# Kernel tuning notes

Measured on AMD Instinct MI355X. Metric: run time of the kernel, lower is better.

The kernel has to match this reference:

```python
import jax, jax.numpy as jnp
import numpy as np

FPS = [32, 64, 128, 256]
SPATIAL = [(32, 32, 32), (16, 16, 16), (8, 8, 8), (4, 4, 4)]
N_FEAT = 512
B = 2
HEAD_DIM = 16
EPS = 1e-5


def setup_inputs() -> dict:
    key = jax.random.key(0)
    ks = iter(jax.random.split(key, 64))
    inp = {}
    for i, (c, (h, w, z)) in enumerate(zip(FPS, SPATIAL)):
        inp[f"x{i}"] = jax.random.normal(next(ks), (B, c, h, w, z), jnp.float32)
        inp[f"f{i}"] = jax.random.normal(next(ks), (N_FEAT, c), jnp.float32)
        inp[f"kv_w{i}"] = jax.random.normal(next(ks), (2 * c, c), jnp.float32) * 0.02
        inp[f"kv_b{i}"] = jnp.zeros((2 * c,), jnp.float32)
        inp[f"proj_w{i}"] = jax.random.normal(next(ks), (c, c), jnp.float32) * 0.02
        inp[f"proj_b{i}"] = jnp.zeros((c,), jnp.float32)
        inp[f"ln_g{i}"] = jnp.ones((c,), jnp.float32)
        inp[f"ln_b{i}"] = jnp.zeros((c,), jnp.float32)
    inp["x4"] = jax.random.normal(next(ks), (B, 320, 2, 2, 2), jnp.float32)
    inp["x5"] = jax.random.normal(next(ks), (B, 320, 1, 1, 1), jnp.float32)
    return inp


def _block(x5d, feat, kv_w, kv_b, proj_w, proj_b, ln_g, ln_b):
    b, c, h, w, z = x5d.shape
    n = h * w * z
    H = c // HEAD_DIM
    # torch's x.view(b, h*w*z, c) is a raw reshape of [b,c,h,w,z] memory
    xq = x5d.reshape(b, n, c)
    N = feat.shape[0]
    f = jnp.broadcast_to(feat[None], (b, N, c))
    kv = f @ kv_w.T + kv_b                     # [b, N, 2c]
    kv = kv.reshape(b, N, 2, H, HEAD_DIM)
    k = kv[:, :, 0].transpose(0, 2, 1, 3)      # [b, H, N, hd]
    v = kv[:, :, 1].transpose(0, 2, 1, 3)      # [b, H, N, hd]
    q = xq.reshape(b, n, H, HEAD_DIM).transpose(0, 2, 1, 3) * (HEAD_DIM ** -0.5)
    attn = jax.nn.softmax(jnp.einsum('bhnd,bhmd->bhnm', q, k), axis=-1)
    o = jnp.einsum('bhnm,bhmd->bhnd', attn, v)
    o = o.transpose(0, 2, 1, 3).reshape(b, n, c)
    o = o @ proj_w.T + proj_b
    y = 0.5 * o + 0.5 * xq
    mu = jnp.mean(y, axis=-1, keepdims=True)
    var = jnp.var(y, axis=-1, keepdims=True)
    y = (y - mu) / jnp.sqrt(var + EPS) * ln_g + ln_b
    return y.reshape(b, c, h, w, z)


def reference(x0, x1, x2, x3, x4, x5, f0, f1, f2, f3,
              kv_w0, kv_b0, proj_w0, proj_b0, ln_g0, ln_b0,
              kv_w1, kv_b1, proj_w1, proj_b1, ln_g1, ln_b1,
              kv_w2, kv_b2, proj_w2, proj_b2, ln_g2, ln_b2,
              kv_w3, kv_b3, proj_w3, proj_b3, ln_g3, ln_b3):
    xs = [x0, x1, x2, x3]
    fs = [f0, f1, f2, f3]
    ps = [(kv_w0, kv_b0, proj_w0, proj_b0, ln_g0, ln_b0),
          (kv_w1, kv_b1, proj_w1, proj_b1, ln_g1, ln_b1),
          (kv_w2, kv_b2, proj_w2, proj_b2, ln_g2, ln_b2),
          (kv_w3, kv_b3, proj_w3, proj_b3, ln_g3, ln_b3)]
    res = [_block(xs[i], fs[i], *ps[i]) for i in range(4)]
    res.append(x4)  # stage 4: i >= 4 -> passthrough
    res.append(x5)  # last stage appended as-is
    return tuple(res)
```

## Files before the change

kernel.cpp:

```cpp
#include <hip/hip_runtime.h>

#define LOG2E 1.44269504088896340736f
#define RHTOT 174080

typedef float v4f __attribute__((ext_vector_type(4)));

struct Params {
  const float* x[4]; const float* f[4]; const float* kvw[4]; const float* kvb[4];
  const float* pw[4]; const float* pb[4]; const float* g[4]; const float* lb[4];
  float* kb[4]; float* ob[4]; float* out[4];
};

__device__ inline v4f fmav(v4f a, v4f b, v4f c) { return a * b + c; }

__global__ __launch_bounds__(256) void kv_all(Params P) {
  int bid = blockIdx.x;
  int s, local;
  if (bid < 8)       { s = 0; local = bid; }
  else if (bid < 24) { s = 1; local = bid - 8; }
  else if (bid < 56) { s = 2; local = bid - 24; }
  else               { s = 3; local = bid - 56; }
  const int C = 32 << s;
  int nt = local & 7, jt = local >> 3;
  int n0 = nt * 64, j0 = jt * 64;
  const float* __restrict__ f = P.f[s];
  const float* __restrict__ w = P.kvw[s];
  __shared__ float fa[64][17];
  __shared__ float wb[64][17];
  int t = threadIdx.x;
  int ti = t & 15, tj = t >> 4;
  float acc[4][4];
  #pragma unroll
  for (int a = 0; a < 4; a++)
    #pragma unroll
    for (int b = 0; b < 4; b++) acc[a][b] = 0.f;

  for (int k0 = 0; k0 < C; k0 += 16) {
    __syncthreads();
    for (int i = t; i < 1024; i += 256) {
      int r = i >> 4, kk = i & 15;
      fa[r][kk] = f[(n0 + r) * C + k0 + kk];
      wb[r][kk] = w[(j0 + r) * C + k0 + kk];
    }
    __syncthreads();
    #pragma unroll
    for (int kk = 0; kk < 16; ++kk) {
      float av[4], bv[4];
      #pragma unroll
      for (int ii = 0; ii < 4; ii++) av[ii] = fa[ti * 4 + ii][kk];
      #pragma unroll
      for (int jj = 0; jj < 4; jj++) bv[jj] = wb[tj * 4 + jj][kk];
      #pragma unroll
      for (int ii = 0; ii < 4; ii++)
        #pragma unroll
        for (int jj = 0; jj < 4; jj++)
          acc[ii][jj] = fmaf(av[ii], bv[jj], acc[ii][jj]);
    }
  }
  const float* __restrict__ bias = P.kvb[s];
  float* kb = P.kb[s];
  #pragma unroll
  for (int ii = 0; ii < 4; ii++) {
    int n = n0 + ti * 4 + ii;
    #pragma unroll
    for (int jj = 0; jj < 4; jj++) {
      int j = j0 + tj * 4 + jj;
      float val = acc[ii][jj] + bias[j];
      if (j < C) {
        kb[(j >> 4) * 16384 + n * 32 + (j & 15)] = val;
      } else {
        int j2 = j - C;
        kb[(j2 >> 4) * 16384 + n * 32 + 16 + (j2 & 15)] = val;
      }
    }
  }
}

template <int C, int H, int ROWS, int RHB>
__device__ void attn_stage(const float* __restrict__ kb, const float* __restrict__ x,
                           float* __restrict__ accP, float* __restrict__ mP,
                           float* __restrict__ lP, int local, int G, int KPG) {
  int HG = H * G;
  int tile = local / HG, r2 = local % HG;
  int head = r2 / G, kg = r2 % G;
  int t = threadIdx.x;
  int row0 = tile * 512 + t;
  if (row0 >= ROWS) return;
  int row1 = row0 + 256;
  bool v1 = row1 < ROWS;
  int rc1 = v1 ? row1 : (ROWS - 1);
  const float* __restrict__ kvh = kb + head * 16384 + (size_t)kg * KPG * 32;

  const float qs = 0.25f * LOG2E;
  const v4f* xa = (const v4f*)(x + (size_t)row0 * C + head * 16);
  const v4f* xb = (const v4f*)(x + (size_t)rc1 * C + head * 16);
  v4f qa0 = xa[0]*qs, qa1 = xa[1]*qs, qa2 = xa[2]*qs, qa3 = xa[3]*qs;
  v4f qb0 = xb[0]*qs, qb1 = xb[1]*qs, qb2 = xb[2]*qs, qb3 = xb[3]*qs;

  float ma = -1e30f, la = 0.f, mb = -1e30f, lb = 0.f;
  v4f aa0 = 0.f, aa1 = 0.f, aa2 = 0.f, aa3 = 0.f;
  v4f ab0 = 0.f, ab1 = 0.f, ab2 = 0.f, ab3 = 0.f;

  #pragma unroll 2
  for (int key = 0; key < KPG; ++key) {
    const v4f* kr = (const v4f*)(kvh + (size_t)key * 32);
    v4f k0 = kr[0], k1 = kr[1], k2 = kr[2], k3 = kr[3];
    v4f ta = qa0 * k0; ta = fmav(qa1, k1, ta); ta = fmav(qa2, k2, ta); ta = fmav(qa3, k3, ta);
    v4f tb = qb0 * k0; tb = fmav(qb1, k1, tb); tb = fmav(qb2, k2, tb); tb = fmav(qb3, k3, tb);
    float sa = (ta.x + ta.y) + (ta.z + ta.w);
    float sb = (tb.x + tb.y) + (tb.z + tb.w);
    if (__any(fmaxf(sa - ma, sb - mb) > 8.f)) {
      float mna = fmaxf(ma, sa);
      float ra = __builtin_amdgcn_exp2f(ma - mna);
      la *= ra; aa0 *= ra; aa1 *= ra; aa2 *= ra; aa3 *= ra; ma = mna;
      float mnb = fmaxf(mb, sb);
      float rb = __builtin_amdgcn_exp2f(mb - mnb);
      lb *= rb; ab0 *= rb; ab1 *= rb; ab2 *= rb; ab3 *= rb; mb = mnb;
    }
    float pa = __builtin_amdgcn_exp2f(sa - ma);
    float pb = __builtin_amdgcn_exp2f(sb - mb);
    la += pa; lb += pb;
    v4f v0 = kr[4], v1_ = kr[5], v2 = kr[6], v3 = kr[7];
    aa0 = fmav(pa, v0, aa0); aa1 = fmav(pa, v1_, aa1);
    aa2 = fmav(pa, v2, aa2); aa3 = fmav(pa, v3, aa3);
    ab0 = fmav(pb, v0, ab0); ab1 = fmav(pb, v1_, ab1);
    ab2 = fmav(pb, v2, ab2); ab3 = fmav(pb, v3, ab3);
  }

  size_t rhA = (size_t)RHB + (size_t)head * ROWS + row0;
  size_t kgo = (size_t)kg * RHTOT;
  if (G == 1) {
    float inv = 1.f / la;
    v4f* d = (v4f*)(accP + rhA * 16);
    d[0] = aa0 * inv; d[1] = aa1 * inv; d[2] = aa2 * inv; d[3] = aa3 * inv;
    if (v1) {
      float invb = 1.f / lb;
      v4f* e = (v4f*)(accP + ((size_t)RHB + (size_t)head * ROWS + row1) * 16);
      e[0] = ab0 * invb; e[1] = ab1 * invb; e[2] = ab2 * invb; e[3] = ab3 * invb;
    }
  } else {
    mP[kgo + rhA] = ma; lP[kgo + rhA] = la;
    v4f* d = (v4f*)(accP + (kgo + rhA) * 16);
    d[0] = aa0; d[1] = aa1; d[2] = aa2; d[3] = aa3;
    if (v1) {
      size_t rhB = (size_t)RHB + (size_t)head * ROWS + row1;
      mP[kgo + rhB] = mb; lP[kgo + rhB] = lb;
      v4f* e = (v4f*)(accP + (kgo + rhB) * 16);
      e[0] = ab0; e[1] = ab1; e[2] = ab2; e[3] = ab3;
    }
  }
}

__global__ __launch_bounds__(256) void attn_split(
    const float* __restrict__ kb0, const float* __restrict__ kb1,
    const float* __restrict__ kb2, const float* __restrict__ kb3,
    const float* __restrict__ x0, const float* __restrict__ x1,
    const float* __restrict__ x2, const float* __restrict__ x3,
    float* __restrict__ accP, float* __restrict__ mP, float* __restrict__ lP,
    int G, int KPG) {
  int bid = blockIdx.x;
  int b0 = 256 * G, b1 = b0 + 64 * G, b2 = b1 + 16 * G;
  if (bid < b0)      attn_stage<32, 2, 65536, 0>(kb0, x0, accP, mP, lP, bid, G, KPG);
  else if (bid < b1) attn_stage<64, 4, 8192, 131072>(kb1, x1, accP, mP, lP, bid - b0, G, KPG);
  else if (bid < b2) attn_stage<128, 8, 1024, 163840>(kb2, x2, accP, mP, lP, bid - b1, G, KPG);
  else               attn_stage<256, 16, 128, 172032>(kb3, x3, accP, mP, lP, bid - b2, G, KPG);
}

__global__ __launch_bounds__(256) void combine_k(float* __restrict__ accP,
                                                 const float* __restrict__ mP,
                                                 const float* __restrict__ lP, int G) {
  size_t rh = (size_t)blockIdx.x * 256 + threadIdx.x;
  if (rh >= RHTOT) return;
  float M = mP[rh];
  for (int g = 1; g < G; ++g) M = fmaxf(M, mP[(size_t)g * RHTOT + rh]);
  float lt = 0.f;
  v4f o0 = 0.f, o1 = 0.f, o2 = 0.f, o3 = 0.f;
  for (int g = 0; g < G; ++g) {
    size_t idx = (size_t)g * RHTOT + rh;
    float w = __builtin_amdgcn_exp2f(mP[idx] - M);
    lt = fmaf(w, lP[idx], lt);
    const v4f* a = (const v4f*)(accP + idx * 16);
    o0 = fmav(w, a[0], o0); o1 = fmav(w, a[1], o1);
    o2 = fmav(w, a[2], o2); o3 = fmav(w, a[3], o3);
  }
  float inv = 1.f / lt;
  v4f* d = (v4f*)(accP + rh * 16);
  d[0] = o0 * inv; d[1] = o1 * inv; d[2] = o2 * inv; d[3] = o3 * inv;
}

__global__ __launch_bounds__(256) void copy_pass(const float4* __restrict__ x4,
                                                 const float4* __restrict__ x5,
                                                 float4* __restrict__ o) {
  int i = blockIdx.x * 256 + threadIdx.x;
  if (i < 1280)      o[i] = x4[i];
  else if (i < 1440) o[i] = x5[i - 1280];
}

template <int C, int ROWS>
__device__ void proj_stage(const Params& P, int s, int tile, float* olds) {
  constexpr int CP = C + 4;
  constexpr int R = 256 / C;
  constexpr int NR = 8;
  constexpr int RB = 2048 / C;
  constexpr int RB4 = RB * 4;
  int r0 = tile * RB;
  int t = threadIdx.x;
  const float4* __restrict__ ob4 = (const float4*)P.ob[s];
  for (int i = t; i < 512; i += 256) {
    int h = i / RB4, rem = i % RB4;
    int row = rem >> 2, d4 = rem & 3;
    float4 v = ob4[((size_t)h * ROWS + r0 + row) * 4 + d4];
    ((float4*)(olds + row * CP + h * 16))[d4] = v;
  }
  __syncthreads();
  int j = t % C, rg = t / C;
  const float* __restrict__ pw = P.pw[s];
  float acc[NR];
  #pragma unroll
  for (int i = 0; i < NR; ++i) acc[i] = 0.f;
  for (int k = 0; k < C; k += 4) {
    float4 w4 = *(const float4*)(pw + (size_t)j * C + k);
    #pragma unroll
    for (int i = 0; i < NR; ++i) {
      float4 o4 = *(const float4*)(olds + (rg + i * R) * CP + k);
      acc[i] = fmaf(o4.x, w4.x, acc[i]);
      acc[i] = fmaf(o4.y, w4.y, acc[i]);
      acc[i] = fmaf(o4.z, w4.z, acc[i]);
      acc[i] = fmaf(o4.w, w4.w, acc[i]);
    }
  }
  __syncthreads();
  float pbj = P.pb[s][j];
  const float* __restrict__ x = P.x[s];
  #pragma unroll
  for (int i = 0; i < NR; ++i) {
    int r = rg + i * R;
    float xv = x[(size_t)(r0 + r) * C + j];
    olds[r * CP + j] = 0.5f * (acc[i] + pbj) + 0.5f * xv;
  }
  __syncthreads();
  int lane = t & 63, wv = t >> 6;
  const float* __restrict__ g = P.g[s];
  const float* __restrict__ lb = P.lb[s];
  float* __restrict__ out = P.out[s];
  #pragma unroll
  for (int rr = 0; rr < RB / 4; ++rr) {
    int r = wv * (RB / 4) + rr;
    float sum = 0.f, sq = 0.f;
    #pragma unroll
    for (int ch = lane; ch < C; ch += 64) {
      float v = olds[r * CP + ch];
      sum += v; sq = fmaf(v, v, sq);
    }
    #pragma unroll
    for (int o = 32; o; o >>= 1) { sum += __shfl_xor(sum, o); sq += __shfl_xor(sq, o); }
    float mu = sum * (1.f / C);
    float var = sq * (1.f / C) - mu * mu;
    float rstd = rsqrtf(var + 1e-5f);
    #pragma unroll
    for (int ch = lane; ch < C; ch += 64) {
      float v = (olds[r * CP + ch] - mu) * rstd;
      out[(size_t)(r0 + r) * C + ch] = fmaf(v, g[ch], lb[ch]);
    }
  }
}

__global__ __launch_bounds__(256) void proj_ln_all(Params P) {
  __shared__ float olds[2304];
  int bid = blockIdx.x;
  if (bid < 1024)      proj_stage<32, 65536>(P, 0, bid, olds);
  else if (bid < 1280) proj_stage<64, 8192>(P, 1, bid - 1024, olds);
  else if (bid < 1344) proj_stage<128, 1024>(P, 2, bid - 1280, olds);
  else                 proj_stage<256, 128>(P, 3, bid - 1344, olds);
}

extern "C" void kernel_launch(void* const* d_in, const int* in_sizes, int n_in,
                              void* d_out, int out_size, void* d_ws, size_t ws_size,
                              hipStream_t stream) {
  Params P;
  float* ws = (float*)d_ws;
  float* out = (float*)d_out;
  const size_t kvoff[4]  = {0, 32768, 98304, 229376};
  const size_t A0 = 491520;
  const size_t rhbase[4] = {0, 131072, 163840, 172032};
  const size_t outoff[4] = {0, 2097152, 2621440, 2752512};

  int G = (ws_size >= (size_t)52101120) ? 4 : 1;
  int KPG = 512 / G;
  float* accP = ws + A0;
  float* mP = accP + (size_t)G * 2785280;
  float* lP = mP + (size_t)G * RHTOT;

  for (int i = 0; i < 4; ++i) {
    const int b = i * 8;
    P.x[i]   = (const float*)d_in[b + 0];
    P.f[i]   = (const float*)d_in[b + 1];
    P.kvw[i] = (const float*)d_in[b + 2];
    P.kvb[i] = (const float*)d_in[b + 3];
    P.pw[i]  = (const float*)d_in[b + 4];
    P.pb[i]  = (const float*)d_in[b + 5];
    P.g[i]   = (const float*)d_in[b + 6];
    P.lb[i]  = (const float*)d_in[b + 7];
    P.kb[i]  = ws + kvoff[i];
    P.ob[i]  = accP + rhbase[i] * 16;
    P.out[i] = out + outoff[i];
  }

  copy_pass<<<6, 256, 0, stream>>>((const float4*)d_in[32], (const float4*)d_in[33],
                                   (float4*)(out + 2785280));
  kv_all<<<120, 256, 0, stream>>>(P);
  attn_split<<<352 * G, 256, 0, stream>>>(P.kb[0], P.kb[1], P.kb[2], P.kb[3],
                                          P.x[0], P.x[1], P.x[2], P.x[3],
                                          accP, mP, lP, G, KPG);
  if (G > 1) combine_k<<<680, 256, 0, stream>>>(accP, mP, lP, G);
  proj_ln_all<<<1360, 256, 0, stream>>>(P);
}
```

Measured before the change: 357.3 us.

## Fuse split-K combine into proj kernel, merge copy into kv, double-buffer K/V loads

Removes the separate copy_pass and combine_k launches: the passthrough copy runs on extra blocks of kv_all, and the split-softmax merge across key groups now happens while proj_ln_all loads its tile into LDS. The attention inner loop explicitly double-buffers the K/V row into registers so the next key's loads are issued before the current key's compute. This saves two launches and one full read/write round trip of the accumulator buffer, at the cost of more register pressure in the attention loop and redundant mP/lP reads per float4 in the projection kernel.

```diff
diff --git a/kernel.cpp b/kernel.cpp
--- a/kernel.cpp
+++ b/kernel.cpp
@@ -8,13 +8,21 @@
 struct Params {
   const float* x[4]; const float* f[4]; const float* kvw[4]; const float* kvb[4];
   const float* pw[4]; const float* pb[4]; const float* g[4]; const float* lb[4];
-  float* kb[4]; float* ob[4]; float* out[4];
+  float* kb[4]; float* out[4];
+  const float4* cx4; const float4* cx5; float4* cout;
 };
 
+__device__ inline v4f fmav(float p, v4f b, v4f c) { return p * b + c; }
 __device__ inline v4f fmav(v4f a, v4f b, v4f c) { return a * b + c; }
 
 __global__ __launch_bounds__(256) void kv_all(Params P) {
   int bid = blockIdx.x;
+  if (bid >= 120) {
+    int i = (bid - 120) * 256 + threadIdx.x;
+    if (i < 1280)      P.cout[i] = P.cx4[i];
+    else if (i < 1440) P.cout[i] = P.cx5[i - 1280];
+    return;
+  }
   int s, local;
   if (bid < 8)       { s = 0; local = bid; }
   else if (bid < 24) { s = 1; local = bid - 8; }
@@ -89,7 +97,7 @@
   int row1 = row0 + 256;
   bool v1 = row1 < ROWS;
   int rc1 = v1 ? row1 : (ROWS - 1);
-  const float* __restrict__ kvh = kb + head * 16384 + (size_t)kg * KPG * 32;
+  const v4f* __restrict__ kvh = (const v4f*)(kb + head * 16384 + (size_t)kg * KPG * 32);
 
   const float qs = 0.25f * LOG2E;
   const v4f* xa = (const v4f*)(x + (size_t)row0 * C + head * 16);
@@ -101,31 +109,46 @@
   v4f aa0 = 0.f, aa1 = 0.f, aa2 = 0.f, aa3 = 0.f;
   v4f ab0 = 0.f, ab1 = 0.f, ab2 = 0.f, ab3 = 0.f;
 
-  #pragma unroll 2
-  for (int key = 0; key < KPG; ++key) {
-    const v4f* kr = (const v4f*)(kvh + (size_t)key * 32);
-    v4f k0 = kr[0], k1 = kr[1], k2 = kr[2], k3 = kr[3];
-    v4f ta = qa0 * k0; ta = fmav(qa1, k1, ta); ta = fmav(qa2, k2, ta); ta = fmav(qa3, k3, ta);
-    v4f tb = qb0 * k0; tb = fmav(qb1, k1, tb); tb = fmav(qb2, k2, tb); tb = fmav(qb3, k3, tb);
-    float sa = (ta.x + ta.y) + (ta.z + ta.w);
-    float sb = (tb.x + tb.y) + (tb.z + tb.w);
-    if (__any(fmaxf(sa - ma, sb - mb) > 8.f)) {
-      float mna = fmaxf(ma, sa);
-      float ra = __builtin_amdgcn_exp2f(ma - mna);
-      la *= ra; aa0 *= ra; aa1 *= ra; aa2 *= ra; aa3 *= ra; ma = mna;
-      float mnb = fmaxf(mb, sb);
-      float rb = __builtin_amdgcn_exp2f(mb - mnb);
-      lb *= rb; ab0 *= rb; ab1 *= rb; ab2 *= rb; ab3 *= rb; mb = mnb;
-    }
-    float pa = __builtin_amdgcn_exp2f(sa - ma);
-    float pb = __builtin_amdgcn_exp2f(sb - mb);
-    la += pa; lb += pb;
-    v4f v0 = kr[4], v1_ = kr[5], v2 = kr[6], v3 = kr[7];
-    aa0 = fmav(pa, v0, aa0); aa1 = fmav(pa, v1_, aa1);
-    aa2 = fmav(pa, v2, aa2); aa3 = fmav(pa, v3, aa3);
-    ab0 = fmav(pb, v0, ab0); ab1 = fmav(pb, v1_, ab1);
-    ab2 = fmav(pb, v2, ab2); ab3 = fmav(pb, v3, ab3);
-  }
+  v4f A[8], B[8];
+
+#define LOADBUF(D, idx) do { const v4f* r_ = kvh + (size_t)(idx) * 8;          \
+    D[0]=r_[0]; D[1]=r_[1]; D[2]=r_[2]; D[3]=r_[3];                            \
+    D[4]=r_[4]; D[5]=r_[5]; D[6]=r_[6]; D[7]=r_[7]; } while (0)
+
+#define STEP(Bf) do {                                                          \
+    v4f ta = qa0*Bf[0]; ta = fmav(qa1,Bf[1],ta);                               \
+    ta = fmav(qa2,Bf[2],ta); ta = fmav(qa3,Bf[3],ta);                          \
+    v4f tb = qb0*Bf[0]; tb = fmav(qb1,Bf[1],tb);                               \
+    tb = fmav(qb2,Bf[2],tb); tb = fmav(qb3,Bf[3],tb);                          \
+    float sa = (ta.x + ta.y) + (ta.z + ta.w);        \
+    float sb = (tb.x + tb.y) + (tb.z + tb.w);                                  \
+    if (__any(fmaxf(sa - ma, sb - mb) > 8.f)) {           \
+      float mna = fmaxf(ma, sa);                                               \
+      float ra = __builtin_amdgcn_exp2f(ma - mna);                             \
+      la *= ra; aa0 *= ra; aa1 *= ra; aa2 *= ra; aa3 *= ra; ma = mna;          \
+      float mnb = fmaxf(mb, sb);                                               \
+      float rb = __builtin_amdgcn_exp2f(mb - mnb);                             \
+      lb *= rb; ab0 *= rb; ab1 *= rb; ab2 *= rb; ab3 *= rb; mb = mnb;          \
+    }                                                                          \
+    float pa = __builtin_amdgcn_exp2f(sa - ma);                                \
+    float pb = __builtin_amdgcn_exp2f(sb - mb);                                \
+    la += pa; lb += pb;                                                        \
+    aa0 = fmav(pa, Bf[4], aa0); aa1 = fmav(pa, Bf[5], aa1);                    \
+    aa2 = fmav(pa, Bf[6], aa2); aa3 = fmav(pa, Bf[7], aa3);                    \
+    ab0 = fmav(pb, Bf[4], ab0); ab1 = fmav(pb, Bf[5], ab1);                    \
+    ab2 = fmav(pb, Bf[6], ab2); ab3 = fmav(pb, Bf[7], ab3); } while (0)
+
+  LOADBUF(A, 0);
+  #pragma unroll 1
+  for (int key = 0; key < KPG; key += 2) {
+    LOADBUF(B, key + 1);
+    STEP(A);
+    int nx = key + 2 < KPG ? key + 2 : 0;
+    LOADBUF(A, nx);
+    STEP(B);
+  }
+#undef LOADBUF
+#undef STEP
 
   size_t rhA = (size_t)RHB + (size_t)head * ROWS + row0;
   size_t kgo = (size_t)kg * RHTOT;
@@ -166,38 +189,10 @@
   else               attn_stage<256, 16, 128, 172032>(kb3, x3, accP, mP, lP, bid - b2, G, KPG);
 }
 
-__global__ __launch_bounds__(256) void combine_k(float* __restrict__ accP,
-                                                 const float* __restrict__ mP,
-                                                 const float* __restrict__ lP, int G) {
-  size_t rh = (size_t)blockIdx.x * 256 + threadIdx.x;
-  if (rh >= RHTOT) return;
-  float M = mP[rh];
-  for (int g = 1; g < G; ++g) M = fmaxf(M, mP[(size_t)g * RHTOT + rh]);
-  float lt = 0.f;
-  v4f o0 = 0.f, o1 = 0.f, o2 = 0.f, o3 = 0.f;
-  for (int g = 0; g < G; ++g) {
-    size_t idx = (size_t)g * RHTOT + rh;
-    float w = __builtin_amdgcn_exp2f(mP[idx] - M);
-    lt = fmaf(w, lP[idx], lt);
-    const v4f* a = (const v4f*)(accP + idx * 16);
-    o0 = fmav(w, a[0], o0); o1 = fmav(w, a[1], o1);
-    o2 = fmav(w, a[2], o2); o3 = fmav(w, a[3], o3);
-  }
-  float inv = 1.f / lt;
-  v4f* d = (v4f*)(accP + rh * 16);
-  d[0] = o0 * inv; d[1] = o1 * inv; d[2] = o2 * inv; d[3] = o3 * inv;
-}
-
-__global__ __launch_bounds__(256) void copy_pass(const float4* __restrict__ x4,
-                                                 const float4* __restrict__ x5,
-                                                 float4* __restrict__ o) {
-  int i = blockIdx.x * 256 + threadIdx.x;
-  if (i < 1280)      o[i] = x4[i];
-  else if (i < 1440) o[i] = x5[i - 1280];
-}
-
-template <int C, int ROWS>
-__device__ void proj_stage(const Params& P, int s, int tile, float* olds) {
+template <int C, int ROWS, int RHB>
+__device__ void proj_stage(const Params& P, int s, int tile, float* olds,
+                           const float* __restrict__ accP, const float* __restrict__ mP,
+                           const float* __restrict__ lP, int G) {
   constexpr int CP = C + 4;
   constexpr int R = 256 / C;
   constexpr int NR = 8;
@@ -205,12 +200,30 @@
   constexpr int RB4 = RB * 4;
   int r0 = tile * RB;
   int t = threadIdx.x;
-  const float4* __restrict__ ob4 = (const float4*)P.ob[s];
+  const float4* __restrict__ a4 = (const float4*)accP;
   for (int i = t; i < 512; i += 256) {
-    int h = i / RB4, rem = i % RB4;
+    int h = i / RB4, rem = i - h * RB4;
     int row = rem >> 2, d4 = rem & 3;
-    float4 v = ob4[((size_t)h * ROWS + r0 + row) * 4 + d4];
-    ((float4*)(olds + row * CP + h * 16))[d4] = v;
+    size_t rh = (size_t)RHB + (size_t)h * ROWS + r0 + row;
+    float4 o;
+    if (G == 1) {
+      o = a4[rh * 4 + d4];
+    } else {
+      float M = mP[rh];
+      for (int g = 1; g < G; ++g) M = fmaxf(M, mP[(size_t)g * RHTOT + rh]);
+      float lt = 0.f;
+      v4f acc = 0.f;
+      for (int g = 0; g < G; ++g) {
+        size_t idx = (size_t)g * RHTOT + rh;
+        float w = __builtin_amdgcn_exp2f(mP[idx] - M);
+        lt = fmaf(w, lP[idx], lt);
+        v4f av = ((const v4f*)accP)[idx * 4 + d4];
+        acc = fmav(w, av, acc);
+      }
+      float inv = 1.f / lt;
+      o.x = acc.x * inv; o.y = acc.y * inv; o.z = acc.z * inv; o.w = acc.w * inv;
+    }
+    ((float4*)(olds + row * CP + h * 16))[d4] = o;
   }
   __syncthreads();
   int j = t % C, rg = t / C;
@@ -265,13 +278,15 @@
   }
 }
 
-__global__ __launch_bounds__(256) void proj_ln_all(Params P) {
+__global__ __launch_bounds__(256) void proj_ln_all(Params P, const float* __restrict__ accP,
+                                                   const float* __restrict__ mP,
+                                                   const float* __restrict__ lP, int G) {
   __shared__ float olds[2304];
   int bid = blockIdx.x;
-  if (bid < 1024)      proj_stage<32, 65536>(P, 0, bid, olds);
-  else if (bid < 1280) proj_stage<64, 8192>(P, 1, bid - 1024, olds);
-  else if (bid < 1344) proj_stage<128, 1024>(P, 2, bid - 1280, olds);
-  else                 proj_stage<256, 128>(P, 3, bid - 1344, olds);
+  if (bid < 1024)      proj_stage<32, 65536, 0>(P, 0, bid, olds, accP, mP, lP, G);
+  else if (bid < 1280) proj_stage<64, 8192, 131072>(P, 1, bid - 1024, olds, accP, mP, lP, G);
+  else if (bid < 1344) proj_stage<128, 1024, 163840>(P, 2, bid - 1280, olds, accP, mP, lP, G);
+  else                 proj_stage<256, 128, 172032>(P, 3, bid - 1344, olds, accP, mP, lP, G);
 }
 
 extern "C" void kernel_launch(void* const* d_in, const int* in_sizes, int n_in,
@@ -282,7 +297,6 @@
   float* out = (float*)d_out;
   const size_t kvoff[4]  = {0, 32768, 98304, 229376};
   const size_t A0 = 491520;
-  const size_t rhbase[4] = {0, 131072, 163840, 172032};
   const size_t outoff[4] = {0, 2097152, 2621440, 2752512};
 
   int G = (ws_size >= (size_t)52101120) ? 4 : 1;
@@ -302,16 +316,15 @@
     P.g[i]   = (const float*)d_in[b + 6];
     P.lb[i]  = (const float*)d_in[b + 7];
     P.kb[i]  = ws + kvoff[i];
-    P.ob[i]  = accP + rhbase[i] * 16;
     P.out[i] = out + outoff[i];
   }
-
-  copy_pass<<<6, 256, 0, stream>>>((const float4*)d_in[32], (const float4*)d_in[33],
-                                   (float4*)(out + 2785280));
-  kv_all<<<120, 256, 0, stream>>>(P);
+  P.cx4 = (const float4*)d_in[32];
+  P.cx5 = (const float4*)d_in[33];
+  P.cout = (float4*)(out + 2785280);
+
+  kv_all<<<126, 256, 0, stream>>>(P);
   attn_split<<<352 * G, 256, 0, stream>>>(P.kb[0], P.kb[1], P.kb[2], P.kb[3],
                                           P.x[0], P.x[1], P.x[2], P.x[3],
                                           accP, mP, lP, G, KPG);
-  if (G > 1) combine_k<<<680, 256, 0, stream>>>(accP, mP, lP, G);
-  proj_ln_all<<<1360, 256, 0, stream>>>(P);
-}
+  proj_ln_all<<<1360, 256, 0, stream>>>(P, accP, mP, lP, G);
+}
```

Result: faster. 294.2 us (-17.7%).
